# Kernel tuning notes

Hardware: AMD Instinct MI355X
Metric: run time of the kernel (lower is better)

Reference implementation:

```python
import jax, jax.numpy as jnp
import numpy as np

B, T, S, D, H, V = 32, 128, 128, 512, 512, 16000

def setup_inputs() -> dict:
    key = jax.random.key(0)
    ks = jax.random.split(key, 12)
    s = 0.02
    return {
        "x": jax.random.randint(ks[0], (B, T), 0, V),
        "teacher": jax.random.randint(ks[1], (B, T), 0, V),
        "z": jax.random.normal(ks[2], (B, S, H), jnp.float32),
        "embed": jax.random.normal(ks[3], (V, D), jnp.float32) * s,
        "W_ih": jax.random.normal(ks[4], (4 * H, D), jnp.float32) * s,
        "b_ih": jnp.zeros((4 * H,), jnp.float32),
        "W_hh": jax.random.normal(ks[5], (4 * H, H), jnp.float32) * s,
        "b_hh": jnp.zeros((4 * H,), jnp.float32),
        "Wq": jax.random.normal(ks[6], (H, H), jnp.float32) * s,
        "Wk": jax.random.normal(ks[7], (H, H), jnp.float32) * s,
        "v_att": jax.random.normal(ks[8], (H,), jnp.float32) * s,
        "W_proj": jax.random.normal(ks[9], (V, 2 * H), jnp.float32) * s,
        "b_proj": jnp.zeros((V,), jnp.float32),
    }

def reference(x, teacher, z, embed, W_ih, b_ih, W_hh, b_hh, Wq, Wk, v_att, W_proj, b_proj):
    # Deterministic path: teacher forcing always on, dropout = identity (eval).
    # Input token at step 0 is x[:,0]; at step i>0 it is teacher[:, i-1].
    tok_seq = jnp.concatenate([x[:, :1], teacher[:, :-1]], axis=1)  # [B,T]
    emb_seq = jnp.transpose(embed[tok_seq], (1, 0, 2))              # [T,B,D]
    keys = jnp.einsum('bsh,kh->bsk', z, Wk.T)                       # precompute attention keys [B,S,H]

    def step(carry, e_t):
        hx, cx = carry
        gates = e_t @ W_ih.T + b_ih + hx @ W_hh.T + b_hh            # [B,4H]
        i, f, g, o = jnp.split(gates, 4, axis=-1)
        i, f, o = jax.nn.sigmoid(i), jax.nn.sigmoid(f), jax.nn.sigmoid(o)
        cx = f * cx + i * jnp.tanh(g)
        hx = o * jnp.tanh(cx)
        # Bahdanau additive attention
        q = hx @ Wq.T                                               # [B,H]
        score = jnp.einsum('bsh,h->bs', jnp.tanh(keys + q[:, None, :]), v_att)
        w = jax.nn.softmax(score, axis=-1)                          # [B,S]
        cxt = jnp.einsum('bs,bsh->bh', w, z)                        # [B,H]
        logits = jnp.concatenate([cxt, hx], axis=-1) @ W_proj.T + b_proj  # [B,V]
        return (hx, cx), logits

    hx0 = jnp.zeros((x.shape[0], W_hh.shape[1]), z.dtype)
    cx0 = jnp.zeros_like(hx0)
    _, logits = jax.lax.scan(step, (hx0, cx0), emb_seq)             # [T,B,V]
    return jnp.transpose(logits, (1, 0, 2))                        # [B,T,V]
```

## Files before the change

### kernel.cpp

```cpp
#include <hip/hip_runtime.h>
#include <hip/hip_bf16.h>
#include <cstddef>

constexpr int B = 32, T = 128, S = 128, D = 512, H = 512, V = 16000;
constexpr int G4H = 4 * H;
constexpr int TB = T * B;

typedef __bf16 bf16x8 __attribute__((ext_vector_type(8)));
typedef float  f32x4  __attribute__((ext_vector_type(4)));

__device__ __forceinline__ float tanh_fast(float x) {
    return 1.0f - 2.0f / (__expf(2.0f * x) + 1.0f);
}
__device__ __forceinline__ float sigmoid_fast(float x) {
    return 1.0f / (1.0f + __expf(-x));
}
__device__ __forceinline__ unsigned short f2bf_rn(float x) {
    unsigned u = __float_as_uint(x);
    unsigned r = (u + 0x7FFFu + ((u >> 16) & 1u)) >> 16;
    return (unsigned short)r;
}
__device__ __forceinline__ float bf2f(unsigned short h) {
    return __uint_as_float(((unsigned)h) << 16);
}
__device__ __forceinline__ void async16(const void* g, void* l) {
    __builtin_amdgcn_global_load_lds(
        (const __attribute__((address_space(1))) void*)g,
        (__attribute__((address_space(3))) void*)l, 16, 0, 0);
}

__global__ __launch_bounds__(128) void gather_emb(
    const int* __restrict__ x, const int* __restrict__ teacher,
    const float* __restrict__ embed, float* __restrict__ emb_g)
{
    int r = blockIdx.x;
    int t = r >> 5, b = r & 31;
    int tok = (t == 0) ? x[b * T] : teacher[b * T + t - 1];
    const float4* src = (const float4*)(embed + (size_t)tok * D);
    float4* dst = (float4*)(emb_g + (size_t)r * D);
    dst[threadIdx.x] = src[threadIdx.x];
}

template<bool BT>
__global__ __launch_bounds__(256) void gemm_kernel(
    const float* __restrict__ A, const float* __restrict__ Bm,
    const float* __restrict__ bias1, const float* __restrict__ bias2,
    float* __restrict__ C, int M, int N, int K)
{
    constexpr int BM = 128, BN = 64, BK = 16;
    __shared__ float As[BK][BM + 4];
    __shared__ float Bs[BK][BN + 4];

    int tid = threadIdx.x;
    int m0 = blockIdx.y * BM, n0 = blockIdx.x * BN;
    int tx = tid & 15, ty = tid >> 4;
    int ar = tid >> 2;
    int ak = (tid & 3) * 4;
    int bkk = tid >> 4;
    int bnn = (tid & 15) * 4;

    float acc[8][4];
    #pragma unroll
    for (int i = 0; i < 8; ++i)
        #pragma unroll
        for (int j = 0; j < 4; ++j) acc[i][j] = 0.f;

    for (int k0 = 0; k0 < K; k0 += BK) {
        #pragma unroll
        for (int rr = 0; rr < 2; ++rr) {
            int row = ar + rr * 64;
            float4 v = *(const float4*)(A + (size_t)(m0 + row) * K + k0 + ak);
            As[ak + 0][row] = v.x; As[ak + 1][row] = v.y;
            As[ak + 2][row] = v.z; As[ak + 3][row] = v.w;
        }
        if (BT) {
            float4 v = *(const float4*)(Bm + (size_t)(n0 + ar) * K + k0 + ak);
            Bs[ak + 0][ar] = v.x; Bs[ak + 1][ar] = v.y;
            Bs[ak + 2][ar] = v.z; Bs[ak + 3][ar] = v.w;
        } else {
            float4 v = *(const float4*)(Bm + (size_t)(k0 + bkk) * N + n0 + bnn);
            *(float4*)&Bs[bkk][bnn] = v;
        }
        __syncthreads();

        #pragma unroll
        for (int kk = 0; kk < BK; ++kk) {
            float a[8], bb[4];
            *(float4*)&a[0] = *(const float4*)&As[kk][ty * 8];
            *(float4*)&a[4] = *(const float4*)&As[kk][ty * 8 + 4];
            *(float4*)&bb[0] = *(const float4*)&Bs[kk][tx * 4];
            #pragma unroll
            for (int i = 0; i < 8; ++i)
                #pragma unroll
                for (int j = 0; j < 4; ++j)
                    acc[i][j] = fmaf(a[i], bb[j], acc[i][j]);
        }
        __syncthreads();
    }

    float bs[4];
    #pragma unroll
    for (int j = 0; j < 4; ++j) {
        float v = 0.f;
        if (bias1) v += bias1[n0 + tx * 4 + j];
        if (bias2) v += bias2[n0 + tx * 4 + j];
        bs[j] = v;
    }
    #pragma unroll
    for (int i = 0; i < 8; ++i) {
        int row = m0 + ty * 8 + i;
        float* crow = C + (size_t)row * N;
        float4 o;
        o.x = acc[i][0] + bs[0]; o.y = acc[i][1] + bs[1];
        o.z = acc[i][2] + bs[2]; o.w = acc[i][3] + bs[3];
        *(float4*)(crow + n0 + tx * 4) = o;
    }
}

__global__ __launch_bounds__(256) void lstm_step2(
    const float* __restrict__ gates_ih_t,
    const float* __restrict__ W_hh,
    const float* __restrict__ Hprev,
    float* __restrict__ Hcur,
    float* __restrict__ cx,
    int first)
{
    __shared__ float part[8][8][32];
    __shared__ float g8[8][32];

    int tid = threadIdx.x, bk = blockIdx.x;
    int b = tid & 31, r = tid >> 5;
    int h0 = bk * 2;

    float acc[8] = {0.f, 0.f, 0.f, 0.f, 0.f, 0.f, 0.f, 0.f};
    if (!first) {
        float4 hreg[16];
        const float4* hp = (const float4*)(Hprev + (size_t)b * 512 + r * 64);
        #pragma unroll
        for (int j = 0; j < 16; ++j) hreg[j] = hp[j];
        #pragma unroll
        for (int rr = 0; rr < 8; ++rr) {
            int row = (rr >> 1) * 512 + h0 + (rr & 1);
            const float4* wp = (const float4*)(W_hh + (size_t)row * 512 + r * 64);
            float a0 = 0.f, a1 = 0.f, a2 = 0.f, a3 = 0.f;
            #pragma unroll
            for (int j = 0; j < 16; ++j) {
                float4 w = wp[j], x = hreg[j];
                a0 = fmaf(w.x, x.x, a0); a1 = fmaf(w.y, x.y, a1);
                a2 = fmaf(w.z, x.z, a2); a3 = fmaf(w.w, x.w, a3);
            }
            acc[rr] = (a0 + a1) + (a2 + a3);
        }
    }
    #pragma unroll
    for (int rr = 0; rr < 8; ++rr) part[r][rr][b] = acc[rr];
    __syncthreads();

    float gate = gates_ih_t[(size_t)b * 2048 + (r >> 1) * 512 + h0 + (r & 1)];
    #pragma unroll
    for (int rs = 0; rs < 8; ++rs) gate += part[rs][r][b];
    g8[r][b] = gate;
    __syncthreads();

    if (tid < 64) {
        int hl = tid >> 5, bb = tid & 31;
        float gi = g8[0 + hl][bb];
        float gf = g8[2 + hl][bb];
        float gg = g8[4 + hl][bb];
        float go = g8[6 + hl][bb];
        float i_ = sigmoid_fast(gi), f_ = sigmoid_fast(gf), o_ = sigmoid_fast(go);
        float c_old = first ? 0.f : cx[(size_t)(h0 + hl) * 32 + bb];
        float c = fmaf(f_, c_old, i_ * tanh_fast(gg));
        cx[(size_t)(h0 + hl) * 32 + bb] = c;
        Hcur[(size_t)bb * 512 + h0 + hl] = o_ * tanh_fast(c);
    }
}

__global__ __launch_bounds__(256) void attn_fused(
    const float* __restrict__ Q, const float* __restrict__ keys,
    const float* __restrict__ z, const float* __restrict__ v_att,
    const float* __restrict__ Hseq, float* __restrict__ U)
{
    __shared__ float qv[512], va[512], ph[256], sc[128], red[128];
    int r = blockIdx.x, b = r & 31, tid = threadIdx.x;

    if (tid < 128) ((float4*)qv)[tid] = ((const float4*)(Q + (size_t)r * H))[tid];
    else           ((float4*)va)[tid - 128] = ((const float4*)v_att)[tid - 128];
    __syncthreads();

    int s = tid >> 1, half = tid & 1;
    const float4* k4 = (const float4*)(keys + ((size_t)b * S + s) * H + half * 256);
    const float4* q4p = (const float4*)(qv + half * 256);
    const float4* v4p = (const float4*)(va + half * 256);
    float acc = 0.f;
    #pragma unroll 4
    for (int i = 0; i < 64; ++i) {
        float4 kv = k4[i], q4 = q4p[i], v4 = v4p[i];
        acc += tanh_fast(kv.x + q4.x) * v4.x + tanh_fast(kv.y + q4.y) * v4.y
             + tanh_fast(kv.z + q4.z) * v4.z + tanh_fast(kv.w + q4.w) * v4.w;
    }
    ph[tid] = acc;
    __syncthreads();
    if (tid < 128) { float v = ph[2 * tid] + ph[2 * tid + 1]; sc[tid] = v; red[tid] = v; }
    __syncthreads();
    for (int st = 64; st > 0; st >>= 1) {
        if (tid < st) red[tid] = fmaxf(red[tid], red[tid + st]);
        __syncthreads();
    }
    float mx = red[0];
    __syncthreads();
    if (tid < 128) { float e = __expf(sc[tid] - mx); sc[tid] = e; red[tid] = e; }
    __syncthreads();
    for (int st = 64; st > 0; st >>= 1) {
        if (tid < st) red[tid] += red[tid + st];
        __syncthreads();
    }
    float inv = 1.0f / red[0];

    const float* zb = z + (size_t)b * S * H;
    int h1 = tid, h2 = tid + 256;
    float c1 = 0.f, c2 = 0.f;
    #pragma unroll 4
    for (int s2 = 0; s2 < S; ++s2) {
        float wgt = sc[s2];
        c1 = fmaf(wgt, zb[(size_t)s2 * H + h1], c1);
        c2 = fmaf(wgt, zb[(size_t)s2 * H + h2], c2);
    }
    float* urow = U + (size_t)r * (2 * H);
    urow[h1] = c1 * inv;
    urow[h2] = c2 * inv;
    urow[H + h1] = Hseq[(size_t)r * H + h1];
    urow[H + h2] = Hseq[(size_t)r * H + h2];
}

__global__ __launch_bounds__(256) void conv_split(
    const float* __restrict__ src, unsigned short* __restrict__ dst, long total4)
{
    for (long i = (long)blockIdx.x * 256 + threadIdx.x; i < total4;
         i += (long)gridDim.x * 256) {
        long rr = i >> 8; int c4 = (int)(i & 255) * 4;
        float4 v = ((const float4*)src)[i];
        ushort4 h, l;
        h.x = f2bf_rn(v.x); l.x = f2bf_rn(v.x - bf2f(h.x));
        h.y = f2bf_rn(v.y); l.y = f2bf_rn(v.y - bf2f(h.y));
        h.z = f2bf_rn(v.z); l.z = f2bf_rn(v.z - bf2f(h.z));
        h.w = f2bf_rn(v.w); l.w = f2bf_rn(v.w - bf2f(h.w));
        *(ushort4*)(dst + rr * 2048 + c4) = h;
        *(ushort4*)(dst + rr * 2048 + 1024 + c4) = l;
    }
}

__global__ __launch_bounds__(256) void gemm_mfma_proj(
    const unsigned short* __restrict__ Ab,
    const unsigned short* __restrict__ Bb,
    const float* __restrict__ bias, float* __restrict__ out)
{
    __shared__ unsigned short As[128 * 32];
    __shared__ unsigned short Bs[128 * 32];

    int tid = threadIdx.x;
    int wid = tid >> 6, lane = tid & 63;
    int wm = wid >> 1, wn = wid & 1;
    int lr = lane & 15, lk = lane >> 4;

    int wg = blockIdx.x;
    int swz = (wg & 7) * 500 + (wg >> 3);
    int m_t = swz & 31, n_t = swz >> 5;
    int m0 = m_t * 128, n0 = n_t * 128;

    f32x4 acc[4][4] = {};

    int crow = lane >> 2;
    int ccol = (lane & 3) * 8;

    for (int kt = 0; kt < 96; ++kt) {
        int k0 = kt * 32;
        int kA = (k0 < 2048) ? k0 : k0 - 2048;
        int kB = (k0 < 1024) ? k0 : k0 - 1024;
        #pragma unroll
        for (int c = 0; c < 2; ++c) {
            int ch = wid * 2 + c;
            int row = ch * 16 + crow;
            const unsigned short* ga = Ab + (size_t)(m0 + row) * 2048 + kA + ccol;
            async16(ga, &As[ch * 512]);
            const unsigned short* gb = Bb + (size_t)(n0 + row) * 2048 + kB + ccol;
            async16(gb, &Bs[ch * 512]);
        }
        __syncthreads();

        bf16x8 a[4], bfr[4];
        #pragma unroll
        for (int f = 0; f < 4; ++f) {
            a[f]   = *(const bf16x8*)&As[(wm * 64 + f * 16 + lr) * 32 + lk * 8];
            bfr[f] = *(const bf16x8*)&Bs[(wn * 64 + f * 16 + lr) * 32 + lk * 8];
        }
        #pragma unroll
        for (int i = 0; i < 4; ++i)
            #pragma unroll
            for (int j = 0; j < 4; ++j)
                acc[i][j] = __builtin_amdgcn_mfma_f32_16x16x32_bf16(
                    a[i], bfr[j], acc[i][j], 0, 0, 0);
        __syncthreads();
    }

    #pragma unroll
    for (int j = 0; j < 4; ++j) {
        int col = n0 + wn * 64 + j * 16 + lr;
        float bv = bias[col];
        #pragma unroll
        for (int i = 0; i < 4; ++i) {
            #pragma unroll
            for (int q = 0; q < 4; ++q) {
                int row = m0 + wm * 64 + i * 16 + lk * 4 + q;
                int t = row >> 5, b = row & 31;
                out[((size_t)b * 128 + t) * 16000 + col] = acc[i][j][q] + bv;
            }
        }
    }
}

extern "C" void kernel_launch(void* const* d_in, const int* in_sizes, int n_in,
                              void* d_out, int out_size, void* d_ws, size_t ws_size,
                              hipStream_t stream)
{
    const int*   x       = (const int*)  d_in[0];
    const int*   teacher = (const int*)  d_in[1];
    const float* z       = (const float*)d_in[2];
    const float* embed   = (const float*)d_in[3];
    const float* W_ih    = (const float*)d_in[4];
    const float* b_ih    = (const float*)d_in[5];
    const float* W_hh    = (const float*)d_in[6];
    const float* b_hh    = (const float*)d_in[7];
    const float* Wq      = (const float*)d_in[8];
    const float* Wk      = (const float*)d_in[9];
    const float* v_att   = (const float*)d_in[10];
    const float* W_proj  = (const float*)d_in[11];
    const float* b_proj  = (const float*)d_in[12];
    float* out = (float*)d_out;

    float* ws = (float*)d_ws;
    float* emb_g    = ws;
    float* gates_ih = ws + 2097152;
    float* keys     = ws + 10485760;
    float* Qbuf     = ws + 12582912;
    float* Hseq     = ws + 14680064;
    float* Ubuf     = ws + 16777216;
    unsigned short* Aconv = (unsigned short*)(ws + 20971520);
    unsigned short* Bconv = (unsigned short*)ws;
    float* cxbuf    = ws + 25165824;

    gather_emb<<<TB, 128, 0, stream>>>(x, teacher, embed, emb_g);

    gemm_kernel<true><<<dim3(G4H / 64, TB / 128), 256, 0, stream>>>(
        emb_g, W_ih, b_ih, b_hh, gates_ih, TB, G4H, D);

    gemm_kernel<false><<<dim3(H / 64, TB / 128), 256, 0, stream>>>(
        z, Wk, nullptr, nullptr, keys, B * S, H, H);

    for (int t = 0; t < T; ++t) {
        const float* hprev = (t == 0) ? nullptr : Hseq + (size_t)(t - 1) * B * H;
        lstm_step2<<<256, 256, 0, stream>>>(
            gates_ih + (size_t)t * B * G4H, W_hh, hprev,
            Hseq + (size_t)t * B * H, cxbuf, t == 0 ? 1 : 0);
    }

    gemm_kernel<true><<<dim3(H / 64, TB / 128), 256, 0, stream>>>(
        Hseq, Wq, nullptr, nullptr, Qbuf, TB, H, H);

    attn_fused<<<TB, 256, 0, stream>>>(Qbuf, keys, z, v_att, Hseq, Ubuf);

    conv_split<<<1024, 256, 0, stream>>>(Ubuf, Aconv, (long)TB * 256);
    conv_split<<<2048, 256, 0, stream>>>(W_proj, Bconv, (long)V * 256);

    gemm_mfma_proj<<<4000, 256, 0, stream>>>(Aconv, Bconv, b_proj, out);
}
```

Baseline: 2.457 ms.

## Replace per-timestep LSTM launches with one persistent per-batch kernel

```diff
diff --git a/kernel.cpp b/kernel.cpp
--- a/kernel.cpp
+++ b/kernel.cpp
@@ -117,62 +117,78 @@
     }
 }
 
-__global__ __launch_bounds__(256) void lstm_step2(
-    const float* __restrict__ gates_ih_t,
-    const float* __restrict__ W_hh,
-    const float* __restrict__ Hprev,
-    float* __restrict__ Hcur,
-    float* __restrict__ cx,
-    int first)
-{
-    __shared__ float part[8][8][32];
-    __shared__ float g8[8][32];
-
-    int tid = threadIdx.x, bk = blockIdx.x;
-    int b = tid & 31, r = tid >> 5;
-    int h0 = bk * 2;
-
-    float acc[8] = {0.f, 0.f, 0.f, 0.f, 0.f, 0.f, 0.f, 0.f};
-    if (!first) {
-        float4 hreg[16];
-        const float4* hp = (const float4*)(Hprev + (size_t)b * 512 + r * 64);
-        #pragma unroll
-        for (int j = 0; j < 16; ++j) hreg[j] = hp[j];
-        #pragma unroll
-        for (int rr = 0; rr < 8; ++rr) {
-            int row = (rr >> 1) * 512 + h0 + (rr & 1);
-            const float4* wp = (const float4*)(W_hh + (size_t)row * 512 + r * 64);
-            float a0 = 0.f, a1 = 0.f, a2 = 0.f, a3 = 0.f;
-            #pragma unroll
-            for (int j = 0; j < 16; ++j) {
-                float4 w = wp[j], x = hreg[j];
-                a0 = fmaf(w.x, x.x, a0); a1 = fmaf(w.y, x.y, a1);
-                a2 = fmaf(w.z, x.z, a2); a3 = fmaf(w.w, x.w, a3);
-            }
-            acc[rr] = (a0 + a1) + (a2 + a3);
-        }
-    }
-    #pragma unroll
-    for (int rr = 0; rr < 8; ++rr) part[r][rr][b] = acc[rr];
-    __syncthreads();
-
-    float gate = gates_ih_t[(size_t)b * 2048 + (r >> 1) * 512 + h0 + (r & 1)];
-    #pragma unroll
-    for (int rs = 0; rs < 8; ++rs) gate += part[rs][r][b];
-    g8[r][b] = gate;
-    __syncthreads();
-
-    if (tid < 64) {
-        int hl = tid >> 5, bb = tid & 31;
-        float gi = g8[0 + hl][bb];
-        float gf = g8[2 + hl][bb];
-        float gg = g8[4 + hl][bb];
-        float go = g8[6 + hl][bb];
-        float i_ = sigmoid_fast(gi), f_ = sigmoid_fast(gf), o_ = sigmoid_fast(go);
-        float c_old = first ? 0.f : cx[(size_t)(h0 + hl) * 32 + bb];
-        float c = fmaf(f_, c_old, i_ * tanh_fast(gg));
-        cx[(size_t)(h0 + hl) * 32 + bb] = c;
-        Hcur[(size_t)bb * 512 + h0 + hl] = o_ * tanh_fast(c);
+__global__ __launch_bounds__(128) void transpose_whh(
+    const float* __restrict__ W, float* __restrict__ WT)
+{
+    int r = blockIdx.x;
+    int g = r >> 9, h = r & 511;
+    const float* src = W + (size_t)r * 512;
+    for (int k = threadIdx.x; k < 512; k += 128)
+        WT[((size_t)k * 512 + h) * 4 + g] = src[k];
+}
+
+__global__ __launch_bounds__(512) void lstm_persist(
+    const float* __restrict__ gates_ih,
+    const float* __restrict__ WT,
+    float* __restrict__ Hseq)
+{
+    __shared__ float hl[512];
+    int b = blockIdx.x, tid = threadIdx.x;
+
+    float c;
+    {
+        const float* gp = gates_ih + (size_t)b * 2048;
+        float gi = gp[tid], gf = gp[512 + tid], gg = gp[1024 + tid], go = gp[1536 + tid];
+        (void)gf;
+        float i_ = sigmoid_fast(gi), o_ = sigmoid_fast(go);
+        c = i_ * tanh_fast(gg);
+        float h = o_ * tanh_fast(c);
+        hl[tid] = h;
+        Hseq[(size_t)b * 512 + tid] = h;
+    }
+    __syncthreads();
+
+    float gi_n, gf_n, gg_n, go_n;
+    {
+        const float* gp = gates_ih + ((size_t)32 + b) * 2048;
+        gi_n = gp[tid]; gf_n = gp[512 + tid]; gg_n = gp[1024 + tid]; go_n = gp[1536 + tid];
+    }
+
+    const f32x4* wp = (const f32x4*)WT + tid;
+
+    for (int t = 1; t < 128; ++t) {
+        f32x4 acc = {gi_n, gf_n, gg_n, go_n};
+        if (t < 127) {
+            const float* gp = gates_ih + ((size_t)(t + 1) * 32 + b) * 2048;
+            gi_n = gp[tid]; gf_n = gp[512 + tid];
+            gg_n = gp[1024 + tid]; go_n = gp[1536 + tid];
+        }
+
+        #pragma unroll 4
+        for (int k4 = 0; k4 < 128; ++k4) {
+            f32x4 h4 = *(const f32x4*)&hl[k4 * 4];
+            f32x4 w0 = wp[(size_t)(k4 * 4 + 0) * 512];
+            f32x4 w1 = wp[(size_t)(k4 * 4 + 1) * 512];
+            f32x4 w2 = wp[(size_t)(k4 * 4 + 2) * 512];
+            f32x4 w3 = wp[(size_t)(k4 * 4 + 3) * 512];
+            acc.x = fmaf(w0.x, h4.x, acc.x); acc.y = fmaf(w0.y, h4.x, acc.y);
+            acc.z = fmaf(w0.z, h4.x, acc.z); acc.w = fmaf(w0.w, h4.x, acc.w);
+            acc.x = fmaf(w1.x, h4.y, acc.x); acc.y = fmaf(w1.y, h4.y, acc.y);
+            acc.z = fmaf(w1.z, h4.y, acc.z); acc.w = fmaf(w1.w, h4.y, acc.w);
+            acc.x = fmaf(w2.x, h4.z, acc.x); acc.y = fmaf(w2.y, h4.z, acc.y);
+            acc.z = fmaf(w2.z, h4.z, acc.z); acc.w = fmaf(w2.w, h4.z, acc.w);
+            acc.x = fmaf(w3.x, h4.w, acc.x); acc.y = fmaf(w3.y, h4.w, acc.y);
+            acc.z = fmaf(w3.z, h4.w, acc.z); acc.w = fmaf(w3.w, h4.w, acc.w);
+        }
+
+        float i_ = sigmoid_fast(acc.x), f_ = sigmoid_fast(acc.y), o_ = sigmoid_fast(acc.w);
+        c = fmaf(f_, c, i_ * tanh_fast(acc.z));
+        float h = o_ * tanh_fast(c);
+
+        __syncthreads();
+        hl[tid] = h;
+        Hseq[((size_t)t * 32 + b) * 512 + tid] = h;
+        __syncthreads();
     }
 }
 
@@ -347,7 +363,9 @@
     float* Ubuf     = ws + 16777216;
     unsigned short* Aconv = (unsigned short*)(ws + 20971520);
     unsigned short* Bconv = (unsigned short*)ws;
-    float* cxbuf    = ws + 25165824;
+    float* WT       = ws + 25165824;
+
+    transpose_whh<<<G4H, 128, 0, stream>>>(W_hh, WT);
 
     gather_emb<<<TB, 128, 0, stream>>>(x, teacher, embed, emb_g);
 
@@ -357,12 +375,7 @@
     gemm_kernel<false><<<dim3(H / 64, TB / 128), 256, 0, stream>>>(
         z, Wk, nullptr, nullptr, keys, B * S, H, H);
 
-    for (int t = 0; t < T; ++t) {
-        const float* hprev = (t == 0) ? nullptr : Hseq + (size_t)(t - 1) * B * H;
-        lstm_step2<<<256, 256, 0, stream>>>(
-            gates_ih + (size_t)t * B * G4H, W_hh, hprev,
-            Hseq + (size_t)t * B * H, cxbuf, t == 0 ? 1 : 0);
-    }
+    lstm_persist<<<B, 512, 0, stream>>>(gates_ih, WT, Hseq);
 
     gemm_kernel<true><<<dim3(H / 64, TB / 128), 256, 0, stream>>>(
         Hseq, Wq, nullptr, nullptr, Qbuf, TB, H, H);
```

Result: slower. 5.329 ms (+116.9%).

## Replace per-step LSTM launches with persistent kernel using grid barrier

Applied to the files above, without the earlier changes.

```diff
diff --git a/kernel.cpp b/kernel.cpp
--- a/kernel.cpp
+++ b/kernel.cpp
@@ -117,62 +117,105 @@
     }
 }
 
-__global__ __launch_bounds__(256) void lstm_step2(
-    const float* __restrict__ gates_ih_t,
+__device__ __forceinline__ void gridbar(unsigned* cnt, unsigned* gen,
+                                        unsigned target, unsigned nblk)
+{
+    __threadfence();
+    __syncthreads();
+    if (threadIdx.x == 0) {
+        unsigned a = __hip_atomic_fetch_add(cnt, 1u, __ATOMIC_RELAXED,
+                                            __HIP_MEMORY_SCOPE_AGENT);
+        if (a == nblk - 1u) {
+            __hip_atomic_store(cnt, 0u, __ATOMIC_RELAXED, __HIP_MEMORY_SCOPE_AGENT);
+            __hip_atomic_store(gen, target, __ATOMIC_RELEASE, __HIP_MEMORY_SCOPE_AGENT);
+        } else {
+            while (__hip_atomic_load(gen, __ATOMIC_RELAXED,
+                                     __HIP_MEMORY_SCOPE_AGENT) < target)
+                __builtin_amdgcn_s_sleep(2);
+        }
+    }
+    __syncthreads();
+    __threadfence();
+}
+
+__global__ __launch_bounds__(256) void lstm_grid(
+    const float* __restrict__ gates_ih,
     const float* __restrict__ W_hh,
-    const float* __restrict__ Hprev,
-    float* __restrict__ Hcur,
-    float* __restrict__ cx,
-    int first)
-{
-    __shared__ float part[8][8][32];
-    __shared__ float g8[8][32];
+    float* __restrict__ Hseq,
+    unsigned* __restrict__ cnt, unsigned* __restrict__ gen)
+{
+    __shared__ float wl[16][512];
+    __shared__ float part[8][16][33];
 
     int tid = threadIdx.x, bk = blockIdx.x;
-    int b = tid & 31, r = tid >> 5;
-    int h0 = bk * 2;
-
-    float acc[8] = {0.f, 0.f, 0.f, 0.f, 0.f, 0.f, 0.f, 0.f};
-    if (!first) {
-        float4 hreg[16];
-        const float4* hp = (const float4*)(Hprev + (size_t)b * 512 + r * 64);
+    int b = tid >> 3, ks = tid & 7;
+    int uhl = tid >> 5, ub = tid & 31;
+    int hg = bk * 4 + uhl;
+
+    for (int i = tid; i < 2048; i += 256) {
+        int lr = i >> 7, k4 = i & 127;
+        int grow = (lr >> 2) * 512 + bk * 4 + (lr & 3);
+        *(float4*)&wl[lr][k4 * 4] = *(const float4*)&W_hh[(size_t)grow * 512 + k4 * 4];
+    }
+
+    float c = 0.f;
+    if (tid < 128) {
+        const float* gp = gates_ih + (size_t)ub * 2048;
+        float gi = gp[hg], gg = gp[1024 + hg], go = gp[1536 + hg];
+        c = sigmoid_fast(gi) * tanh_fast(gg);
+        Hseq[(size_t)ub * 512 + hg] = sigmoid_fast(go) * tanh_fast(c);
+    }
+    __syncthreads();
+
+    for (int t = 1; t < 128; ++t) {
+        float gi = 0.f, gf = 0.f, gg = 0.f, go = 0.f;
+        if (tid < 128) {
+            const float* gp = gates_ih + ((size_t)t * 32 + ub) * 2048;
+            gi = gp[hg]; gf = gp[512 + hg]; gg = gp[1024 + hg]; go = gp[1536 + hg];
+        }
+
+        gridbar(cnt, gen, (unsigned)t, 128u);
+
+        f32x4 hreg[16];
+        const f32x4* hp = (const f32x4*)(Hseq + ((size_t)(t - 1) * 32 + b) * 512 + ks * 64);
         #pragma unroll
         for (int j = 0; j < 16; ++j) hreg[j] = hp[j];
-        #pragma unroll
-        for (int rr = 0; rr < 8; ++rr) {
-            int row = (rr >> 1) * 512 + h0 + (rr & 1);
-            const float4* wp = (const float4*)(W_hh + (size_t)row * 512 + r * 64);
-            float a0 = 0.f, a1 = 0.f, a2 = 0.f, a3 = 0.f;
+
+        float acc[16];
+        #pragma unroll
+        for (int r = 0; r < 16; ++r) acc[r] = 0.f;
+        #pragma unroll
+        for (int j = 0; j < 16; ++j) {
+            f32x4 h4 = hreg[j];
             #pragma unroll
-            for (int j = 0; j < 16; ++j) {
-                float4 w = wp[j], x = hreg[j];
-                a0 = fmaf(w.x, x.x, a0); a1 = fmaf(w.y, x.y, a1);
-                a2 = fmaf(w.z, x.z, a2); a3 = fmaf(w.w, x.w, a3);
+            for (int r = 0; r < 16; ++r) {
+                f32x4 w4 = *(const f32x4*)&wl[r][ks * 64 + j * 4];
+                acc[r] = fmaf(w4.x, h4.x, acc[r]);
+                acc[r] = fmaf(w4.y, h4.y, acc[r]);
+                acc[r] = fmaf(w4.z, h4.z, acc[r]);
+                acc[r] = fmaf(w4.w, h4.w, acc[r]);
             }
-            acc[rr] = (a0 + a1) + (a2 + a3);
-        }
-    }
-    #pragma unroll
-    for (int rr = 0; rr < 8; ++rr) part[r][rr][b] = acc[rr];
-    __syncthreads();
-
-    float gate = gates_ih_t[(size_t)b * 2048 + (r >> 1) * 512 + h0 + (r & 1)];
-    #pragma unroll
-    for (int rs = 0; rs < 8; ++rs) gate += part[rs][r][b];
-    g8[r][b] = gate;
-    __syncthreads();
-
-    if (tid < 64) {
-        int hl = tid >> 5, bb = tid & 31;
-        float gi = g8[0 + hl][bb];
-        float gf = g8[2 + hl][bb];
-        float gg = g8[4 + hl][bb];
-        float go = g8[6 + hl][bb];
-        float i_ = sigmoid_fast(gi), f_ = sigmoid_fast(gf), o_ = sigmoid_fast(go);
-        float c_old = first ? 0.f : cx[(size_t)(h0 + hl) * 32 + bb];
-        float c = fmaf(f_, c_old, i_ * tanh_fast(gg));
-        cx[(size_t)(h0 + hl) * 32 + bb] = c;
-        Hcur[(size_t)bb * 512 + h0 + hl] = o_ * tanh_fast(c);
+        }
+        #pragma unroll
+        for (int r = 0; r < 16; ++r) part[ks][r][b] = acc[r];
+        __syncthreads();
+
+        if (tid < 128) {
+            float s[4];
+            #pragma unroll
+            for (int g = 0; g < 4; ++g) {
+                int lr = g * 4 + uhl;
+                s[g] = ((part[0][lr][ub] + part[1][lr][ub])
+                      + (part[2][lr][ub] + part[3][lr][ub]))
+                     + ((part[4][lr][ub] + part[5][lr][ub])
+                      + (part[6][lr][ub] + part[7][lr][ub]));
+            }
+            float i_ = sigmoid_fast(gi + s[0]);
+            float f_ = sigmoid_fast(gf + s[1]);
+            float o_ = sigmoid_fast(go + s[3]);
+            c = fmaf(f_, c, i_ * tanh_fast(gg + s[2]));
+            Hseq[((size_t)t * 32 + ub) * 512 + hg] = o_ * tanh_fast(c);
+        }
     }
 }
 
@@ -347,7 +390,9 @@
     float* Ubuf     = ws + 16777216;
     unsigned short* Aconv = (unsigned short*)(ws + 20971520);
     unsigned short* Bconv = (unsigned short*)ws;
-    float* cxbuf    = ws + 25165824;
+    unsigned* bar   = (unsigned*)(ws + 25165824);
+
+    hipMemsetAsync(bar, 0, 2 * sizeof(unsigned), stream);
 
     gather_emb<<<TB, 128, 0, stream>>>(x, teacher, embed, emb_g);
 
@@ -357,12 +402,7 @@
     gemm_kernel<false><<<dim3(H / 64, TB / 128), 256, 0, stream>>>(
         z, Wk, nullptr, nullptr, keys, B * S, H, H);
 
-    for (int t = 0; t < T; ++t) {
-        const float* hprev = (t == 0) ? nullptr : Hseq + (size_t)(t - 1) * B * H;
-        lstm_step2<<<256, 256, 0, stream>>>(
-            gates_ih + (size_t)t * B * G4H, W_hh, hprev,
-            Hseq + (size_t)t * B * H, cxbuf, t == 0 ? 1 : 0);
-    }
+    lstm_grid<<<128, 256, 0, stream>>>(gates_ih, W_hh, Hseq, bar, bar + 1);
 
     gemm_kernel<true><<<dim3(H / 64, TB / 128), 256, 0, stream>>>(
         Hseq, Wq, nullptr, nullptr, Qbuf, TB, H, H);
```

Result: slower. 6.365 ms (+159.0%).
